# Performance work log

Measured on AMD Instinct MI355X. Metric: run time of the kernel, lower is better.

Reference implementation:

```python
import jax, jax.numpy as jnp
import numpy as np

B, N, DIM = 2, 2048, 1024
HEADS, DIM_HEAD = 16, 64
INNER = HEADS * DIM_HEAD  # 1024


def setup_inputs() -> dict:
    key = jax.random.key(0)
    k1, k2, k3, k4 = jax.random.split(key, 4)
    x = jax.random.normal(k1, (B, N, DIM), dtype=jnp.float32)
    # Linear weights (stored as [in, out] so y = x @ W)
    Wq = jax.random.normal(k2, (DIM, INNER), dtype=jnp.float32) * (DIM ** -0.5)
    Wkv = jax.random.normal(k3, (DIM, INNER * 2), dtype=jnp.float32) * (DIM ** -0.5)
    Wo = jax.random.normal(k4, (INNER, DIM), dtype=jnp.float32) * (INNER ** -0.5)
    return {"x": x, "Wq": Wq, "Wkv": Wkv, "Wo": Wo}


def reference(x, Wq, Wkv, Wo):
    # q/k/v projections (no bias), split heads: b n (h d) -> b h n d
    b, n, _ = x.shape
    q = (x @ Wq).reshape(b, n, HEADS, DIM_HEAD).transpose(0, 2, 1, 3)
    kv = x @ Wkv
    k, v = jnp.split(kv, 2, axis=-1)
    k = k.reshape(b, n, HEADS, DIM_HEAD).transpose(0, 2, 1, 3)
    v = v.reshape(b, n, HEADS, DIM_HEAD).transpose(0, 2, 1, 3)

    scale = DIM_HEAD ** -0.5
    scores = jnp.einsum('bhid,bhjd->bhij', q, k) * scale  # [b,h,n,n]
    # causal mask: positions j > i masked with most-negative value (as in torch impl)
    max_neg = -jnp.finfo(scores.dtype).max
    causal_mask = jnp.triu(jnp.ones((n, n), dtype=bool), k=1)
    scores = jnp.where(causal_mask, max_neg, scores)
    p = jax.nn.softmax(scores, axis=-1)
    out = jnp.einsum('bhij,bhjd->bhid', p, v)  # [b,h,n,d]
    out = out.transpose(0, 2, 1, 3).reshape(b, n, INNER)
    return out @ Wo
```

## Files before the change

kernel.cpp:

```cpp
#include <hip/hip_runtime.h>
#include <cstdint>


typedef __bf16 bf16_t;
typedef __bf16 bf16x8 __attribute__((ext_vector_type(8)));
typedef __bf16 bf16x4 __attribute__((ext_vector_type(4)));
typedef float  f32x4  __attribute__((ext_vector_type(4)));
typedef float  f32x16 __attribute__((ext_vector_type(16)));
typedef unsigned int u32;

#define QSCALE 0.18033688011112042f


__device__ __forceinline__ float fast_exp2(float x) {
#if __has_builtin(__builtin_amdgcn_exp2f)
  return __builtin_amdgcn_exp2f(x);
#else
  return exp2f(x);
#endif
}

__device__ __forceinline__ void swap32(u32& a, u32& b) {
#if __has_builtin(__builtin_amdgcn_permlane32_swap)
  typedef unsigned int u32x2 __attribute__((ext_vector_type(2)));
  const u32x2 r = __builtin_amdgcn_permlane32_swap(a, b, false, false);
  a = r[0]; b = r[1];
#else
  const u32 xa = (u32)__shfl_xor((int)a, 32, 64);
  const u32 xb = (u32)__shfl_xor((int)b, 32, 64);
  const bool hi = (threadIdx.x & 32) != 0;
  const u32 r0 = hi ? xb : a;
  const u32 r1 = hi ? b : xa;
  a = r0; b = r1;
#endif
}

__device__ __forceinline__ void gload_lds16(const void* gsrc, void* ldst) {
  __builtin_amdgcn_global_load_lds(
      (__attribute__((address_space(1))) void*)(uintptr_t)gsrc,
      (__attribute__((address_space(3))) void*)(uintptr_t)(uint32_t)(uintptr_t)ldst,
      16, 0, 0);
}

__device__ __forceinline__ u32 pkbf(float a, float b) {
  const u32 lo = (u32)__builtin_bit_cast(unsigned short, (bf16_t)a);
  const u32 hi = (u32)__builtin_bit_cast(unsigned short, (bf16_t)b);
  return (hi << 16) | lo;
}

__global__ __launch_bounds__(256) void cvt_kernel(const float* __restrict__ in,
                                                  bf16_t* __restrict__ out) {
  const int idx = (blockIdx.x * 256 + threadIdx.x) * 4;
  const float4 v = *(const float4*)(in + idx);
  bf16x4 o;
  o[0] = (bf16_t)v.x; o[1] = (bf16_t)v.y; o[2] = (bf16_t)v.z; o[3] = (bf16_t)v.w;
  *(bf16x4*)(out + idx) = o;
}

__global__ __launch_bounds__(256) void transpose_kernel(const float* __restrict__ W,
                                                        bf16_t* __restrict__ Wt,
                                                        int K, int Nn) {
  __shared__ float tile[32][33];
  const int bx = blockIdx.x, by = blockIdx.y;
  const int x = bx * 32 + threadIdx.x;
  #pragma unroll
  for (int r0 = 0; r0 < 32; r0 += 8) {
    const int r = r0 + threadIdx.y;
    tile[r][threadIdx.x] = W[(size_t)(by * 32 + r) * Nn + x];
  }
  __syncthreads();
  const int xo = by * 32 + threadIdx.x;
  #pragma unroll
  for (int r0 = 0; r0 < 32; r0 += 8) {
    const int r = r0 + threadIdx.y;
    Wt[(size_t)(bx * 32 + r) * K + xo] = (bf16_t)tile[threadIdx.x][r];
  }
}

template <int MODE>
__global__ __launch_bounds__(256) void gemm_kernel(
    const bf16_t* __restrict__ A, const bf16_t* __restrict__ Bt,
    bf16_t* __restrict__ outQ, bf16_t* __restrict__ outK,
    bf16_t* __restrict__ outV, float* __restrict__ outf) {
  constexpr int KD = 1024;
  __shared__ bf16_t As[2][128][64];
  __shared__ bf16_t Bs[2][128][64];
  const int t = threadIdx.x;
  const int lane = t & 63, w = t >> 6;
  const int wr = w >> 1, wc = w & 1;
  const int lrow = lane & 15, lq = lane >> 4;
  const int bm = blockIdx.y * 128, bn = blockIdx.x * 128;

  f32x4 acc[4][4] = {};

  auto stage = [&](int buf, int k0) {
    #pragma unroll
    for (int i = 0; i < 4; ++i) {
      const int lin = i * 256 + t;
      const int row = lin >> 3;
      const int sc = (lin & 7) ^ (row & 7);
      gload_lds16(A + (size_t)(bm + row) * KD + k0 + sc * 8,
                  &As[buf][0][0] + lin * 8);
      gload_lds16(Bt + (size_t)(bn + row) * KD + k0 + sc * 8,
                  &Bs[buf][0][0] + lin * 8);
    }
  };

  stage(0, 0);
  for (int kt = 0; kt < KD / 64; ++kt) {
    const int cur = kt & 1;
    if (kt + 1 < KD / 64) {
      stage(cur ^ 1, (kt + 1) * 64);
      asm volatile("s_waitcnt vmcnt(8)" ::: "memory");
    } else {
      asm volatile("s_waitcnt vmcnt(0)" ::: "memory");
    }
    __builtin_amdgcn_s_barrier();

    #pragma unroll
    for (int kk = 0; kk < 2; ++kk) {
      bf16x8 aF[4], bF[4];
      #pragma unroll
      for (int m = 0; m < 4; ++m) {
        const int row = wr * 64 + m * 16 + lrow;
        const int ch = (kk * 4 + lq) ^ (row & 7);
        aF[m] = *(const bf16x8*)&As[cur][row][ch * 8];
      }
      #pragma unroll
      for (int n = 0; n < 4; ++n) {
        const int row = wc * 64 + n * 16 + lrow;
        const int ch = (kk * 4 + lq) ^ (row & 7);
        bF[n] = *(const bf16x8*)&Bs[cur][row][ch * 8];
      }
      #pragma unroll
      for (int m = 0; m < 4; ++m)
        #pragma unroll
        for (int n = 0; n < 4; ++n)
          acc[m][n] = __builtin_amdgcn_mfma_f32_16x16x32_bf16(aF[m], bF[n],
                                                              acc[m][n], 0, 0, 0);
    }
    asm volatile("s_waitcnt lgkmcnt(0)" ::: "memory");
    __builtin_amdgcn_s_barrier();
  }

  #pragma unroll
  for (int m = 0; m < 4; ++m) {
    const int ri = bm + wr * 64 + m * 16 + lq * 4;
    #pragma unroll
    for (int n = 0; n < 4; ++n) {
      const int ci = bn + wc * 64 + n * 16 + lrow;
      const f32x4 v = acc[m][n];
      if (MODE == 2) {
        #pragma unroll
        for (int r = 0; r < 4; ++r)
          outf[(size_t)(ri + r) * 1024 + ci] = v[r];
      } else {
        if (ci < 2048) {
          const int cc = ci & 1023;
          const int h = cc >> 6, d = cc & 63;
          bf16_t* dst = (ci < 1024) ? outQ : outK;
          const float sc = (ci < 1024) ? QSCALE : 1.0f;
          const int fpart = (d >> 4) * 2;
          const int lpart = ((d >> 3) & 1) * 32;
          const int epart = d & 7;
          #pragma unroll
          for (int r = 0; r < 4; ++r) {
            const int i = ri + r;
            const int b = i >> 11, q = i & 2047;
            const size_t elem = (size_t)(b * 16 + h) * 131072
                + (size_t)((q >> 6) * 8 + fpart + ((q >> 5) & 1)) * 512
                + (lpart + (q & 31)) * 8 + epart;
            dst[elem] = (bf16_t)(v[r] * sc);
          }
        } else {
          const int hd = ci - 2048;
          const int h = hd >> 6, d = hd & 63;
          const int b = ri >> 11, j0 = ri & 2047;
          bf16x4 pk;
          pk[0] = (bf16_t)v[0]; pk[1] = (bf16_t)v[1];
          pk[2] = (bf16_t)v[2]; pk[3] = (bf16_t)v[3];
          const size_t elem = (size_t)(b * 16 + h) * 131072
              + (size_t)((j0 >> 6) * 8 + ((j0 & 63) >> 4) * 2 + (d >> 5)) * 512
              + ((((j0 >> 3) & 1) * 32) + (d & 31)) * 8 + (j0 & 7);
          *(bf16x4*)(outV + elem) = pk;
        }
      }
    }
  }
}

__global__ void __attribute__((amdgpu_flat_work_group_size(256, 256),
                               amdgpu_waves_per_eu(4, 4)))
attn_kernel(
    const bf16_t* __restrict__ Qf, const bf16_t* __restrict__ Kf,
    const bf16_t* __restrict__ Vf, bf16_t* __restrict__ Ow) {
  const int t = threadIdx.x;
  const int lane = t & 63, w = t >> 6;
  const int l31 = lane & 31, hi = lane >> 5;
  const int G = ((blockIdx.x & 7) << 7) + (blockIdx.x >> 3);
  const int bh = G >> 5;
  const int p = G & 31;
  const int qsA = 63 - p, qsB = p;
  const int ntA = (qsA >> 1) + 1, ntB = (qsB >> 1) + 1;
  const int wA = min(3, (4 * ntA + ((ntA + ntB) >> 1)) / (ntA + ntB));
  const bool isA = (w < wA);
  const int qs = isA ? qsA : qsB;
  const int nt = isA ? ntA : ntB;
  const int widx = isA ? w : (w - wA);
  const int ws = isA ? wA : (4 - wA);
  const int qg = qs * 32 + l31;
  const bf16_t* Qb = Qf + (size_t)bh * 131072 + (size_t)(qs >> 1) * 4096 + (qs & 1) * 512;
  const bf16_t* Kb = Kf + (size_t)bh * 131072;
  const bf16_t* Vb = Vf + (size_t)bh * 131072;

  bf16x8 qf[4];
  #pragma unroll
  for (int ks = 0; ks < 4; ++ks)
    qf[ks] = *(const bf16x8*)(Qb + ks * 1024 + lane * 8);

  f32x16 acc0 = {}, acc1 = {};
  float m_run = -1e30f, l_half = 0.f;

  for (int jt = widx; jt < nt; jt += ws) {
    const bf16_t* Kt = Kb + (size_t)jt * 4096;
    const bf16_t* Vt = Vb + (size_t)jt * 4096;

    bf16x8 kc[8];
    #pragma unroll
    for (int f = 0; f < 8; ++f)
      kc[f] = *(const bf16x8*)(Kt + f * 512 + lane * 8);

    f32x16 st0 = {}, st1 = {};
    #pragma unroll
    for (int ks = 0; ks < 4; ++ks) {
      st0 = __builtin_amdgcn_mfma_f32_32x32x16_bf16(kc[2 * ks], qf[ks], st0, 0, 0, 0);
      st1 = __builtin_amdgcn_mfma_f32_32x32x16_bf16(kc[2 * ks + 1], qf[ks], st1, 0, 0, 0);
    }

    if (jt == nt - 1) {
      const int thr = qg - jt * 64;
      #pragma unroll
      for (int r = 0; r < 16; ++r) {
        const int jl = (r & 3) + 8 * (r >> 2) + 4 * hi;
        st0[r] = (jl > thr) ? -1e30f : st0[r];
        st1[r] = (32 + jl > thr) ? -1e30f : st1[r];
      }
    }

    float t8[8];
    #pragma unroll
    for (int i = 0; i < 8; ++i)
      t8[i] = fmaxf(fmaxf(st0[i], st0[i + 8]), fmaxf(st1[i], st1[i + 8]));
    #pragma unroll
    for (int i = 0; i < 4; ++i) t8[i] = fmaxf(t8[i], t8[i + 4]);
    const float pmax = fmaxf(fmaxf(t8[0], t8[1]), fmaxf(t8[2], t8[3]));

    if (!__all(pmax <= m_run + 8.0f)) {
      const float mx = fmaxf(pmax, __shfl_xor(pmax, 32, 64));
      const float m_new = fmaxf(m_run, mx);
      const float corr = fast_exp2(m_run - m_new);
      m_run = m_new;
      l_half *= corr;
      #pragma unroll
      for (int r = 0; r < 16; ++r) { acc0[r] *= corr; acc1[r] *= corr; }
    }

    #pragma unroll
    for (int r = 0; r < 16; ++r) {
      st0[r] = fast_exp2(st0[r] - m_run);
      st1[r] = fast_exp2(st1[r] - m_run);
    }
    float s8[8];
    #pragma unroll
    for (int i = 0; i < 8; ++i)
      s8[i] = (st0[i] + st0[i + 8]) + (st1[i] + st1[i + 8]);
    #pragma unroll
    for (int i = 0; i < 4; ++i) s8[i] += s8[i + 4];
    l_half += (s8[0] + s8[1]) + (s8[2] + s8[3]);

    bf16x8 vf[8];
    #pragma unroll
    for (int f = 0; f < 8; ++f)
      vf[f] = *(const bf16x8*)(Vt + f * 512 + lane * 8);

    u32 Wa[8], Wb[8];
    #pragma unroll
    for (int g = 0; g < 8; ++g) {
      Wa[g] = pkbf(st0[2 * g], st0[2 * g + 1]);
      Wb[g] = pkbf(st1[2 * g], st1[2 * g + 1]);
    }
    swap32(Wa[0], Wa[2]); swap32(Wa[1], Wa[3]);
    swap32(Wa[4], Wa[6]); swap32(Wa[5], Wa[7]);
    swap32(Wb[0], Wb[2]); swap32(Wb[1], Wb[3]);
    swap32(Wb[4], Wb[6]); swap32(Wb[5], Wb[7]);
    const uint4 u0 = make_uint4(Wa[0], Wa[1], Wa[2], Wa[3]);
    const uint4 u1 = make_uint4(Wa[4], Wa[5], Wa[6], Wa[7]);
    const uint4 u2 = make_uint4(Wb[0], Wb[1], Wb[2], Wb[3]);
    const uint4 u3 = make_uint4(Wb[4], Wb[5], Wb[6], Wb[7]);
    const bf16x8 pf0 = __builtin_bit_cast(bf16x8, u0);
    const bf16x8 pf1 = __builtin_bit_cast(bf16x8, u1);
    const bf16x8 pf2 = __builtin_bit_cast(bf16x8, u2);
    const bf16x8 pf3 = __builtin_bit_cast(bf16x8, u3);

    #pragma unroll
    for (int tt = 0; tt < 4; ++tt) {
      const bf16x8 pf = tt == 0 ? pf0 : tt == 1 ? pf1 : tt == 2 ? pf2 : pf3;
      acc0 = __builtin_amdgcn_mfma_f32_32x32x16_bf16(vf[2 * tt], pf, acc0, 0, 0, 0);
      acc1 = __builtin_amdgcn_mfma_f32_32x32x16_bf16(vf[2 * tt + 1], pf, acc1, 0, 0, 0);
    }
  }

  const float l_wave = l_half + __shfl_xor(l_half, 32, 64);

  __shared__ float mO[2][32][64];
  __shared__ float mML[2][2][64];
  const bool leader = (w == 0) || (w == wA);
  if (!leader) {
    const int slot = isA ? (w - 1) : (wA - 1 + (w - wA - 1));
    mML[0][slot][lane] = m_run;
    mML[1][slot][lane] = l_wave;
    #pragma unroll
    for (int r = 0; r < 16; ++r) {
      mO[slot][r][lane] = acc0[r];
      mO[slot][16 + r][lane] = acc1[r];
    }
  }
  __syncthreads();
  if (leader) {
    const int base = isA ? 0 : (wA - 1);
    const int nsl = ws - 1;
    float mk[2], lk[2], ck[2];
    float mt = m_run;
    for (int k = 0; k < nsl; ++k) {
      mk[k] = mML[0][base + k][lane];
      lk[k] = mML[1][base + k][lane];
      mt = fmaxf(mt, mk[k]);
    }
    const float c0 = fast_exp2(m_run - mt);
    float l = l_wave * c0;
    for (int k = 0; k < nsl; ++k) {
      ck[k] = fast_exp2(mk[k] - mt);
      l += lk[k] * ck[k];
    }
    const float inv = 1.0f / l;
    const int b = bh >> 4, h = bh & 15;
    bf16_t* Obase = Ow + (((size_t)(b * 2048 + qg)) << 10) + h * 64;
    #pragma unroll
    for (int g = 0; g < 4; ++g) {
      bf16x4 p0, p1;
      #pragma unroll
      for (int j = 0; j < 4; ++j) {
        float a0 = acc0[4 * g + j] * c0;
        float a1 = acc1[4 * g + j] * c0;
        for (int k = 0; k < nsl; ++k) {
          a0 += mO[base + k][4 * g + j][lane] * ck[k];
          a1 += mO[base + k][16 + 4 * g + j][lane] * ck[k];
        }
        p0[j] = (bf16_t)(a0 * inv);
        p1[j] = (bf16_t)(a1 * inv);
      }
      *(bf16x4*)(Obase + 8 * g + 4 * hi) = p0;
      *(bf16x4*)(Obase + 32 + 8 * g + 4 * hi) = p1;
    }
  }
}

extern "C" void kernel_launch(void* const* d_in, const int* in_sizes, int n_in,
                              void* d_out, int out_size, void* d_ws, size_t ws_size,
                              hipStream_t stream) {
  const float* x   = (const float*)d_in[0];
  const float* Wq  = (const float*)d_in[1];
  const float* Wkv = (const float*)d_in[2];
  const float* Wo  = (const float*)d_in[3];
  float* out = (float*)d_out;
  char* ws = (char*)d_ws;

  const size_t MB = 1024 * 1024;
  bf16_t* Xbf   = (bf16_t*)(ws);
  bf16_t* Wqkvt = (bf16_t*)(ws + 8 * MB);
  bf16_t* Wot   = (bf16_t*)(ws + 14 * MB);
  bf16_t* Qw    = (bf16_t*)(ws + 16 * MB);
  bf16_t* Kw    = (bf16_t*)(ws + 24 * MB);
  bf16_t* Vtw   = (bf16_t*)(ws + 32 * MB);
  bf16_t* Aw    = (bf16_t*)(ws + 40 * MB);

  cvt_kernel<<<4096, 256, 0, stream>>>(x, Xbf);
  dim3 tb(32, 8);
  transpose_kernel<<<dim3(32, 32), tb, 0, stream>>>(Wq, Wqkvt, 1024, 1024);
  transpose_kernel<<<dim3(64, 32), tb, 0, stream>>>(Wkv, Wqkvt + 1024 * 1024, 1024, 2048);
  transpose_kernel<<<dim3(32, 32), tb, 0, stream>>>(Wo, Wot, 1024, 1024);

  gemm_kernel<1><<<dim3(24, 32), 256, 0, stream>>>(Xbf, Wqkvt, Qw, Kw, Vtw, nullptr);
  attn_kernel<<<1024, 256, 0, stream>>>(Qw, Kw, Vtw, Aw);
  gemm_kernel<2><<<dim3(8, 32), 256, 0, stream>>>(Aw, Wot, nullptr, nullptr, nullptr, out);
}
```

Before: 107.4 us.

## Stage Q/K epilogue through LDS and narrow output GEMM tile to 64

The QKV GEMM epilogue for Q and K now writes the scaled bf16 tile into shared memory in the attention-friendly fragment layout, then copies contiguous 16-byte chunks to global memory instead of scattered 2-byte stores. The output projection GEMM is templated on column tile width and launched with 64-wide tiles, doubling the block count to 512 for better CU occupancy on a grid that previously had only 256 blocks. The narrower tile lowers per-block reuse of A and adds a barrier plus LDS traffic to the epilogue.

```diff
diff --git a/kernel.cpp b/kernel.cpp
--- a/kernel.cpp
+++ b/kernel.cpp
@@ -77,21 +77,24 @@
   }
 }
 
-template <int MODE>
+template <int MODE, int BN>
 __global__ __launch_bounds__(256) void gemm_kernel(
     const bf16_t* __restrict__ A, const bf16_t* __restrict__ Bt,
     bf16_t* __restrict__ outQ, bf16_t* __restrict__ outK,
     bf16_t* __restrict__ outV, float* __restrict__ outf) {
   constexpr int KD = 1024;
+  constexpr int NB = BN / 32;
+  constexpr int NW = BN / 2;
+  constexpr int NACC = NW / 16;
   __shared__ bf16_t As[2][128][64];
-  __shared__ bf16_t Bs[2][128][64];
+  __shared__ bf16_t Bs[2][BN][64];
   const int t = threadIdx.x;
   const int lane = t & 63, w = t >> 6;
   const int wr = w >> 1, wc = w & 1;
   const int lrow = lane & 15, lq = lane >> 4;
-  const int bm = blockIdx.y * 128, bn = blockIdx.x * 128;
-
-  f32x4 acc[4][4] = {};
+  const int bm = blockIdx.y * 128, bn = blockIdx.x * BN;
+
+  f32x4 acc[4][NACC] = {};
 
   auto stage = [&](int buf, int k0) {
     #pragma unroll
@@ -101,6 +104,12 @@
       const int sc = (lin & 7) ^ (row & 7);
       gload_lds16(A + (size_t)(bm + row) * KD + k0 + sc * 8,
                   &As[buf][0][0] + lin * 8);
+    }
+    #pragma unroll
+    for (int i = 0; i < NB; ++i) {
+      const int lin = i * 256 + t;
+      const int row = lin >> 3;
+      const int sc = (lin & 7) ^ (row & 7);
       gload_lds16(Bt + (size_t)(bn + row) * KD + k0 + sc * 8,
                   &Bs[buf][0][0] + lin * 8);
     }
@@ -111,7 +120,10 @@
     const int cur = kt & 1;
     if (kt + 1 < KD / 64) {
       stage(cur ^ 1, (kt + 1) * 64);
-      asm volatile("s_waitcnt vmcnt(8)" ::: "memory");
+      if constexpr (BN == 128)
+        asm volatile("s_waitcnt vmcnt(8)" ::: "memory");
+      else
+        asm volatile("s_waitcnt vmcnt(6)" ::: "memory");
     } else {
       asm volatile("s_waitcnt vmcnt(0)" ::: "memory");
     }
@@ -119,7 +131,7 @@
 
     #pragma unroll
     for (int kk = 0; kk < 2; ++kk) {
-      bf16x8 aF[4], bF[4];
+      bf16x8 aF[4], bF[NACC];
       #pragma unroll
       for (int m = 0; m < 4; ++m) {
         const int row = wr * 64 + m * 16 + lrow;
@@ -127,15 +139,15 @@
         aF[m] = *(const bf16x8*)&As[cur][row][ch * 8];
       }
       #pragma unroll
-      for (int n = 0; n < 4; ++n) {
-        const int row = wc * 64 + n * 16 + lrow;
+      for (int n = 0; n < NACC; ++n) {
+        const int row = wc * NW + n * 16 + lrow;
         const int ch = (kk * 4 + lq) ^ (row & 7);
         bF[n] = *(const bf16x8*)&Bs[cur][row][ch * 8];
       }
       #pragma unroll
       for (int m = 0; m < 4; ++m)
         #pragma unroll
-        for (int n = 0; n < 4; ++n)
+        for (int n = 0; n < NACC; ++n)
           acc[m][n] = __builtin_amdgcn_mfma_f32_16x16x32_bf16(aF[m], bF[n],
                                                               acc[m][n], 0, 0, 0);
     }
@@ -143,47 +155,74 @@
     __builtin_amdgcn_s_barrier();
   }
 
-  #pragma unroll
-  for (int m = 0; m < 4; ++m) {
-    const int ri = bm + wr * 64 + m * 16 + lq * 4;
-    #pragma unroll
-    for (int n = 0; n < 4; ++n) {
-      const int ci = bn + wc * 64 + n * 16 + lrow;
-      const f32x4 v = acc[m][n];
-      if (MODE == 2) {
+  if constexpr (MODE == 2) {
+    #pragma unroll
+    for (int m = 0; m < 4; ++m) {
+      const int ri = bm + wr * 64 + m * 16 + lq * 4;
+      #pragma unroll
+      for (int n = 0; n < NACC; ++n) {
+        const int ci = bn + wc * NW + n * 16 + lrow;
+        const f32x4 v = acc[m][n];
         #pragma unroll
         for (int r = 0; r < 4; ++r)
           outf[(size_t)(ri + r) * 1024 + ci] = v[r];
-      } else {
-        if (ci < 2048) {
-          const int cc = ci & 1023;
-          const int h = cc >> 6, d = cc & 63;
-          bf16_t* dst = (ci < 1024) ? outQ : outK;
-          const float sc = (ci < 1024) ? QSCALE : 1.0f;
-          const int fpart = (d >> 4) * 2;
-          const int lpart = ((d >> 3) & 1) * 32;
-          const int epart = d & 7;
-          #pragma unroll
-          for (int r = 0; r < 4; ++r) {
-            const int i = ri + r;
-            const int b = i >> 11, q = i & 2047;
-            const size_t elem = (size_t)(b * 16 + h) * 131072
-                + (size_t)((q >> 6) * 8 + fpart + ((q >> 5) & 1)) * 512
-                + (lpart + (q & 31)) * 8 + epart;
-            dst[elem] = (bf16_t)(v[r] * sc);
-          }
-        } else {
-          const int hd = ci - 2048;
-          const int h = hd >> 6, d = hd & 63;
-          const int b = ri >> 11, j0 = ri & 2047;
-          bf16x4 pk;
-          pk[0] = (bf16_t)v[0]; pk[1] = (bf16_t)v[1];
-          pk[2] = (bf16_t)v[2]; pk[3] = (bf16_t)v[3];
-          const size_t elem = (size_t)(b * 16 + h) * 131072
-              + (size_t)((j0 >> 6) * 8 + ((j0 & 63) >> 4) * 2 + (d >> 5)) * 512
-              + ((((j0 >> 3) & 1) * 32) + (d & 31)) * 8 + (j0 & 7);
-          *(bf16x4*)(outV + elem) = pk;
+      }
+    }
+  } else if (bn < 2048) {
+    bf16_t* Cs = (bf16_t*)&As[0][0][0];
+    bf16_t* dst = (bn < 1024) ? outQ : outK;
+    const float sc = (bn < 1024) ? QSCALE : 1.0f;
+    #pragma unroll
+    for (int m = 0; m < 4; ++m) {
+      const int rr0 = wr * 64 + m * 16 + lq * 4;
+      #pragma unroll
+      for (int n = 0; n < NACC; ++n) {
+        const int c = wc * NW + n * 16 + lrow;
+        const int hh = c >> 6, d = c & 63;
+        const f32x4 v = acc[m][n];
+        #pragma unroll
+        for (int r = 0; r < 4; ++r) {
+          const int rr = rr0 + r;
+          const int off = ((hh * 2 + (rr >> 6)) << 12)
+                        + (((d >> 4) * 2 + ((rr >> 5) & 1)) << 9)
+                        + ((((d >> 3) & 1) * 32 + (rr & 31)) << 3) + (d & 7);
+          Cs[off] = (bf16_t)(v[r] * sc);
         }
+      }
+    }
+    __syncthreads();
+    const int b = bm >> 11;
+    const int qc0 = (bm & 2047) >> 6;
+    const int h0 = (bn & 1023) >> 6;
+    #pragma unroll
+    for (int chk = 0; chk < 4; ++chk) {
+      const int hh = chk >> 1, qc = chk & 1;
+      bf16_t* gb = dst + (size_t)(b * 16 + h0 + hh) * 131072
+                 + (size_t)(qc0 + qc) * 4096;
+      #pragma unroll
+      for (int it = 0; it < 2; ++it) {
+        const int e = (it * 256 + t) * 8;
+        *(bf16x8*)(gb + e) = *(const bf16x8*)(Cs + chk * 4096 + e);
+      }
+    }
+  } else {
+    #pragma unroll
+    for (int m = 0; m < 4; ++m) {
+      const int ri = bm + wr * 64 + m * 16 + lq * 4;
+      #pragma unroll
+      for (int n = 0; n < NACC; ++n) {
+        const int ci = bn + wc * NW + n * 16 + lrow;
+        const f32x4 v = acc[m][n];
+        const int hd = ci - 2048;
+        const int h = hd >> 6, d = hd & 63;
+        const int b = ri >> 11, j0 = ri & 2047;
+        bf16x4 pk;
+        pk[0] = (bf16_t)v[0]; pk[1] = (bf16_t)v[1];
+        pk[2] = (bf16_t)v[2]; pk[3] = (bf16_t)v[3];
+        const size_t elem = (size_t)(b * 16 + h) * 131072
+            + (size_t)((j0 >> 6) * 8 + ((j0 & 63) >> 4) * 2 + (d >> 5)) * 512
+            + ((((j0 >> 3) & 1) * 32) + (d & 31)) * 8 + (j0 & 7);
+        *(bf16x4*)(outV + elem) = pk;
       }
     }
   }
@@ -390,7 +429,7 @@
   transpose_kernel<<<dim3(64, 32), tb, 0, stream>>>(Wkv, Wqkvt + 1024 * 1024, 1024, 2048);
   transpose_kernel<<<dim3(32, 32), tb, 0, stream>>>(Wo, Wot, 1024, 1024);
 
-  gemm_kernel<1><<<dim3(24, 32), 256, 0, stream>>>(Xbf, Wqkvt, Qw, Kw, Vtw, nullptr);
+  gemm_kernel<1, 128><<<dim3(24, 32), 256, 0, stream>>>(Xbf, Wqkvt, Qw, Kw, Vtw, nullptr);
   attn_kernel<<<1024, 256, 0, stream>>>(Qw, Kw, Vtw, Aw);
-  gemm_kernel<2><<<dim3(8, 32), 256, 0, stream>>>(Aw, Wot, nullptr, nullptr, nullptr, out);
-}
+  gemm_kernel<2, 64><<<dim3(16, 32), 256, 0, stream>>>(Aw, Wot, nullptr, nullptr, nullptr, out);
+}
```

Measured after the change: 101.8 us. 1.06x faster.
